# Kernel tuning notes

Hardware: AMD Instinct MI355X
Metric: run time of the kernel (lower is better)

The kernel has to match this reference:

```python
import jax, jax.numpy as jnp
import numpy as np

N_NODES = 50000
N_EDGES = 800000
IN_DIM = 128
HIDDEN = 128
OUT_DIM = 128


def setup_inputs() -> dict:
    key = jax.random.key(0)
    ks = jax.random.split(key, 16)
    s = 0.05
    inp = {
        "x": jax.random.normal(ks[0], (N_NODES, IN_DIM), jnp.float32),
        "edge_index": jax.random.randint(ks[1], (2, N_EDGES), 0, N_NODES, jnp.int64),
        "batch": jax.random.randint(ks[2], (25000,), 0, N_NODES, jnp.int64),
        "labels": jax.random.randint(ks[3], (N_NODES,), 0, 2, jnp.int64),
        # SAGEConv layer 1: in->hidden
        "W1l": jax.random.normal(ks[4], (HIDDEN, IN_DIM), jnp.float32) * s,
        "b1": jnp.zeros((HIDDEN,), jnp.float32),
        "W1r": jax.random.normal(ks[5], (HIDDEN, IN_DIM), jnp.float32) * s,
        # SAGEConv layer 2: hidden->hidden
        "W2l": jax.random.normal(ks[6], (HIDDEN, HIDDEN), jnp.float32) * s,
        "b2": jnp.zeros((HIDDEN,), jnp.float32),
        "W2r": jax.random.normal(ks[7], (HIDDEN, HIDDEN), jnp.float32) * s,
        # SAGEConv layer 3: hidden->out
        "W3l": jax.random.normal(ks[8], (OUT_DIM, HIDDEN), jnp.float32) * s,
        "b3": jnp.zeros((OUT_DIM,), jnp.float32),
        "W3r": jax.random.normal(ks[9], (OUT_DIM, HIDDEN), jnp.float32) * s,
        # classifier head: out->2
        "Wlin": jax.random.normal(ks[10], (2, OUT_DIM), jnp.float32) * s,
        "blin": jnp.zeros((2,), jnp.float32),
    }
    return inp


def _sage_conv(h, src, dst, Wl, bl, Wr):
    # mean aggregation of source features at destination nodes
    msg = h[src]                                            # [E, d]
    ssum = jax.ops.segment_sum(msg, dst, num_segments=N_NODES)
    cnt = jax.ops.segment_sum(jnp.ones((src.shape[0], 1), h.dtype), dst,
                              num_segments=N_NODES)
    agg = ssum / jnp.maximum(cnt, 1.0)
    # lin_l(agg) + lin_r(h): aggregate-then-transform (same math, cheaper)
    return agg @ Wl.T + bl + h @ Wr.T


def reference(x, edge_index, batch, labels,
              W1l, b1, W1r, W2l, b2, W2r, W3l, b3, W3r, Wlin, blin):
    src, dst = edge_index[0], edge_index[1]
    h = jax.nn.relu(_sage_conv(x, src, dst, W1l, b1, W1r))
    h = jax.nn.relu(_sage_conv(h, src, dst, W2l, b2, W2r))
    h = _sage_conv(h, src, dst, W3l, b3, W3r)               # no act after last
    preds = jax.nn.softmax(h @ Wlin.T + blin, axis=1)       # nn.Softmax(dim=1)
    # CrossEntropyLoss on (already-softmaxed) preds, as in the original module
    logp = jax.nn.log_softmax(preds[batch], axis=1)
    loss = -jnp.mean(jnp.take_along_axis(logp, labels[batch][:, None], axis=1))
    return loss
```

## Files before the change

### kernel.cpp

```cpp
#include <hip/hip_runtime.h>
#include <hip/hip_bf16.h>

#define N_NODES 50000
#define MPAD    50048
#define N_EDGES 800000
#define DIM     128
#define N_BATCH 25000
#define NBUCK   196
#define BCAP    8192
#define NBIN    64

typedef unsigned short u16;
typedef unsigned int   u32;
typedef unsigned char  u8;
typedef unsigned long long u64;

typedef __attribute__((ext_vector_type(8))) short bf16x8;
typedef __attribute__((ext_vector_type(4))) float f32x4;
typedef __attribute__((ext_vector_type(2))) float f32x2;

static __device__ __forceinline__ float bf2f(u16 u) {
    union { u32 i; float f; } v; v.i = ((u32)u) << 16; return v.f;
}
static __device__ __forceinline__ u16 f2bf(float f) {
    union { float f; u32 i; } v; v.f = f;
    u32 x = v.i;
    u32 r = x + 0x7fffu + ((x >> 16) & 1u);
    return (u16)(r >> 16);
}
template <bool HI>
static __device__ __forceinline__ u32 pk8(float a, float b, u32 old) {
    return (u32)__builtin_amdgcn_cvt_pk_fp8_f32(a, b, (int)old, HI);
}


__global__ void k_init(int* bcur, float* accum, int* hcount, u8* mask,
                       int* c1g, int* c3g, int* o1g, int* o3g) {
    int gid = blockIdx.x * 256 + threadIdx.x;
    if (gid < NBUCK) bcur[gid] = gid * BCAP;
    if (gid < NBIN) { c1g[gid] = 0; c3g[gid] = 0; o1g[gid] = 0; o3g[gid] = 0; }
    if (gid < N_NODES) mask[gid] = 0;
    if (gid == 0) { accum[0] = 0.f; hcount[0] = 0; }
}


#define SB_PART 196
#define SB_CX   3324
#define SB_CW   3708
#define SB_MK   3806

__global__ __launch_bounds__(256) void k_setup(
    const int* __restrict__ src, const int* __restrict__ dst,
    int* __restrict__ bcur, u64* __restrict__ ebuf,
    const float* __restrict__ x, u16* __restrict__ xb, u8* __restrict__ x8,
    const float* __restrict__ W1l, const float* __restrict__ W1r,
    const float* __restrict__ W2l, const float* __restrict__ W2r,
    const float* __restrict__ W3l, const float* __restrict__ W3r,
    u16* __restrict__ wout,
    const int* __restrict__ batch, u8* __restrict__ mask) {
    __shared__ int hist[NBUCK];
    __shared__ int lbase[NBUCK];
    __shared__ int gdelta[NBUCK];
    __shared__ u64 stage[4096];
    __shared__ int gaddr[4096];
    int bid = blockIdx.x;
    int t = threadIdx.x;

    if (bid < SB_PART) {
        for (int i = t; i < NBUCK; i += 256) hist[i] = 0;
        __syncthreads();

        int base = bid * 4096;
        int cnt = N_EDGES - base; if (cnt > 4096) cnt = 4096; if (cnt < 0) cnt = 0;

        int es[16], ed[16], rr[16];
#pragma unroll
        for (int k = 0; k < 16; ++k) {
            int i = t + (k << 8);
            bool ok = i < cnt;
            int e = ok ? (base + i) : 0;
            int s = src[e], d = dst[e];
            es[k] = s; ed[k] = d;
            int r = -1;
            if (ok) r = atomicAdd(&hist[d >> 8], 1);
            rr[k] = r;
        }
        __syncthreads();

        if (t < 64) {
            int run = 0;
            for (int c = 0; c < 4; ++c) {
                int idx = c * 64 + t;
                int v = (idx < NBUCK) ? hist[idx] : 0;
                int orig = v;
                for (int off = 1; off < 64; off <<= 1) {
                    int u = __shfl_up(v, off);
                    if (t >= off) v += u;
                }
                int tot = __shfl(v, 63);
                if (idx < NBUCK) lbase[idx] = run + v - orig;
                run += tot;
            }
        }
        __syncthreads();

        if (t < NBUCK) {
            int c = hist[t];
            int g = atomicAdd(&bcur[t], c);
            gdelta[t] = g - lbase[t];
        }
        __syncthreads();

#pragma unroll
        for (int k = 0; k < 16; ++k) {
            if (rr[k] >= 0) {
                int b = ed[k] >> 8;
                int slot = lbase[b] + rr[k];
                stage[slot] = (((u64)(u32)ed[k]) << 32) | (u32)es[k];
                gaddr[slot] = gdelta[b] + slot;
            }
        }
        __syncthreads();

        for (int i = t; i < cnt; i += 256) {
            ebuf[gaddr[i]] = stage[i];
        }
    } else if (bid < SB_CX) {
        int gid = (bid - SB_PART) * 256 + t;
        int row = gid >> 4;
        int c8  = (gid & 15) << 3;
        u32 outw[4];
        u32 w0 = 0, w1 = 0;
        if (row < N_NODES) {
            const float4* p = (const float4*)(x + (size_t)row * DIM + c8);
            float4 v0 = p[0], v1 = p[1];
            outw[0] = (u32)f2bf(v0.x) | ((u32)f2bf(v0.y) << 16);
            outw[1] = (u32)f2bf(v0.z) | ((u32)f2bf(v0.w) << 16);
            outw[2] = (u32)f2bf(v1.x) | ((u32)f2bf(v1.y) << 16);
            outw[3] = (u32)f2bf(v1.z) | ((u32)f2bf(v1.w) << 16);
            w0 = pk8<false>(v0.x, v0.y, 0); w0 = pk8<true>(v0.z, v0.w, w0);
            w1 = pk8<false>(v1.x, v1.y, 0); w1 = pk8<true>(v1.z, v1.w, w1);
        } else {
            outw[0] = outw[1] = outw[2] = outw[3] = 0;
        }
        *(uint4*)(xb + (size_t)row * DIM + c8) = *(uint4*)outw;
        uint2 o8; o8.x = w0; o8.y = w1;
        *(uint2*)(x8 + (size_t)row * DIM + c8) = o8;
    } else if (bid < SB_CW) {
        int i = (bid - SB_CX) * 256 + t;
        int mat = i >> 14, off = i & 16383;
        const float* s = (mat == 0) ? W1l : (mat == 1) ? W1r : (mat == 2) ? W2l
                       : (mat == 3) ? W2r : (mat == 4) ? W3l : W3r;
        wout[i] = f2bf(s[off]);
    } else {
        int s = (bid - SB_CW) * 256 + t;
        if (s < N_BATCH) mask[batch[s]] = 1;
    }
}


__global__ __launch_bounds__(256) void k_build(const u64* __restrict__ ebuf,
                                               const int* __restrict__ bcur,
                                               const u8* __restrict__ mask,
                                               int* __restrict__ row_ptr,
                                               int* __restrict__ deg,
                                               float* __restrict__ deg_inv,
                                               int* __restrict__ csr_src,
                                               int* __restrict__ c1g,
                                               int* __restrict__ c3g) {
    __shared__ int cnt256[256];
    __shared__ int sh[256];
    __shared__ int cur[256];
    __shared__ int bh1[NBIN];
    __shared__ int bh3[NBIN];
    __shared__ int shbase;
    int b  = blockIdx.x;
    int t  = threadIdx.x;
    int n0 = b << 8;
    cnt256[t] = 0;
    if (t < NBIN) { bh1[t] = 0; bh3[t] = 0; }
    if (t < 64) {
        int s = 0;
        for (int i = t; i < b; i += 64) s += bcur[i] - i * BCAP;
#pragma unroll
        for (int off = 32; off > 0; off >>= 1) s += __shfl_xor(s, off);
        if (t == 0) shbase = s;
    }
    __syncthreads();
    int bbase = shbase;

    int cnt = bcur[b] - b * BCAP;
    const u64* eb = ebuf + (size_t)b * BCAP;
    for (int i = t; i < cnt; i += 256) {
        int d = (int)(eb[i] >> 32);
        atomicAdd(&cnt256[d - n0], 1);
    }
    __syncthreads();

    int myc = cnt256[t];
    sh[t] = myc;
    __syncthreads();
    for (int off = 1; off < 256; off <<= 1) {
        int x = (t >= off) ? sh[t - off] : 0;
        __syncthreads();
        sh[t] += x;
        __syncthreads();
    }
    int rp = bbase + sh[t] - myc;
    int n  = n0 + t;
    if (n < N_NODES) {
        row_ptr[n] = rp;
        deg[n]     = myc;
        deg_inv[n] = 1.0f / (float)(myc < 1 ? 1 : myc);
        int bin = myc < NBIN ? myc : NBIN - 1;
        atomicAdd(&bh1[bin], 1);
        if (mask[n]) atomicAdd(&bh3[bin], 1);
    }
    cur[t] = rp;
    __syncthreads();

    for (int i = t; i < cnt; i += 256) {
        u64 p = eb[i];
        int d = (int)(p >> 32);
        int s = (int)(u32)p;
        int pos = atomicAdd(&cur[d - n0], 1);
        csr_src[pos] = s;
    }
    __syncthreads();
    if (t < NBIN) {
        if (bh1[t]) atomicAdd(&c1g[t], bh1[t]);
        if (bh3[t]) atomicAdd(&c3g[t], bh3[t]);
    }
}


__global__ __launch_bounds__(256) void k_dscatter(const int* __restrict__ deg,
                                                  const u8* __restrict__ mask,
                                                  const int* __restrict__ c1g,
                                                  const int* __restrict__ c3g,
                                                  int* __restrict__ o1g,
                                                  int* __restrict__ o3g,
                                                  int* __restrict__ wl1,
                                                  int* __restrict__ wl3,
                                                  int* __restrict__ n3) {
    __shared__ int bh1[NBIN], bh3[NBIN], bb1[NBIN], bb3[NBIN];
    int t = threadIdx.x;
    int n = blockIdx.x * 256 + t;
    if (t < NBIN) { bh1[t] = 0; bh3[t] = 0; }
    __syncthreads();
    bool valid = n < N_NODES;
    int d = 0, r1 = -1, r3 = -1;
    if (valid) {
        d = deg[n]; if (d >= NBIN) d = NBIN - 1;
        r1 = atomicAdd(&bh1[d], 1);
        if (mask[n]) r3 = atomicAdd(&bh3[d], 1);
    }
    __syncthreads();
    if (t < 64) {
        int v1 = c1g[t], v3 = c3g[t];
        int i1 = v1, i3 = v3;
        for (int off = 1; off < 64; off <<= 1) {
            int u1 = __shfl_up(i1, off);
            int u3 = __shfl_up(i3, off);
            if (t >= off) { i1 += u1; i3 += u3; }
        }
        int res1 = atomicAdd(&o1g[t], bh1[t]);
        int res3 = atomicAdd(&o3g[t], bh3[t]);
        bb1[t] = (i1 - v1) + res1;
        bb3[t] = (i3 - v3) + res3;
        if (blockIdx.x == 0 && t == 63) n3[0] = i3;
    }
    __syncthreads();
    if (valid) {
        wl1[bb1[d] + r1] = n;
        if (r3 >= 0) wl3[bb3[d] + r3] = n;
    }
}


template <bool RELU, bool PRUNED, bool W8>
__global__ __launch_bounds__(256) void k_sage(
    const u16* __restrict__ h, const u8* __restrict__ h8,
    const int* __restrict__ csr_src,
    const int* __restrict__ row_ptr, const int* __restrict__ deg,
    const float* __restrict__ deg_inv,
    const int* __restrict__ wl, const int* __restrict__ wlN,
    const u16* __restrict__ Wl, const u16* __restrict__ Wr,
    const float* __restrict__ bias, u16* __restrict__ out,
    u8* __restrict__ out8) {
    __shared__ u16 tile[16 * 128];
    __shared__ int wlid[16];
    int nwl = PRUNED ? wlN[0] : N_NODES;
    int m0  = blockIdx.x * 16;
    if (m0 >= nwl) return;

    int t    = threadIdx.x;
    int lane = t & 63;
    int wid  = t >> 6;
    int sub  = lane & 15;
    int grp  = lane >> 4;
    int nloc = (wid << 2) + grp;
    int gb   = lane & 48;
    int node = (m0 + nloc < nwl) ? wl[m0 + nloc] : -1;
    if (sub == 0) wlid[nloc] = node;

    float a0 = 0, a1 = 0, a2 = 0, a3 = 0, a4 = 0, a5 = 0, a6 = 0, a7 = 0;

#define ACC8(r) { f32x2 p; \
    p = __builtin_amdgcn_cvt_pk_f32_fp8((r).x, false); a0 += p[0]; a1 += p[1]; \
    p = __builtin_amdgcn_cvt_pk_f32_fp8((r).x, true);  a2 += p[0]; a3 += p[1]; \
    p = __builtin_amdgcn_cvt_pk_f32_fp8((r).y, false); a4 += p[0]; a5 += p[1]; \
    p = __builtin_amdgcn_cvt_pk_f32_fp8((r).y, true);  a6 += p[0]; a7 += p[1]; }

    if (node >= 0) {
        int start = row_ptr[node];
        int cnt   = deg[node];
        for (int c0 = 0; c0 < cnt; c0 += 16) {
            int rem = cnt - c0; if (rem > 16) rem = 16;
            int sidx = 0;
            if (sub < rem) sidx = csr_src[start + c0 + sub];
            int j = 0;
            for (; j + 8 <= rem; j += 8) {
                int i0 = __shfl(sidx, gb + j);
                int i1 = __shfl(sidx, gb + j + 1);
                int i2 = __shfl(sidx, gb + j + 2);
                int i3 = __shfl(sidx, gb + j + 3);
                int i4 = __shfl(sidx, gb + j + 4);
                int i5 = __shfl(sidx, gb + j + 5);
                int i6 = __shfl(sidx, gb + j + 6);
                int i7 = __shfl(sidx, gb + j + 7);
                uint2 r0 = *(const uint2*)(h8 + (size_t)i0 * DIM + sub * 8);
                uint2 r1 = *(const uint2*)(h8 + (size_t)i1 * DIM + sub * 8);
                uint2 r2 = *(const uint2*)(h8 + (size_t)i2 * DIM + sub * 8);
                uint2 r3 = *(const uint2*)(h8 + (size_t)i3 * DIM + sub * 8);
                uint2 r4 = *(const uint2*)(h8 + (size_t)i4 * DIM + sub * 8);
                uint2 r5 = *(const uint2*)(h8 + (size_t)i5 * DIM + sub * 8);
                uint2 r6 = *(const uint2*)(h8 + (size_t)i6 * DIM + sub * 8);
                uint2 r7 = *(const uint2*)(h8 + (size_t)i7 * DIM + sub * 8);
                ACC8(r0); ACC8(r1); ACC8(r2); ACC8(r3);
                ACC8(r4); ACC8(r5); ACC8(r6); ACC8(r7);
            }
            for (; j + 4 <= rem; j += 4) {
                int i0 = __shfl(sidx, gb + j);
                int i1 = __shfl(sidx, gb + j + 1);
                int i2 = __shfl(sidx, gb + j + 2);
                int i3 = __shfl(sidx, gb + j + 3);
                uint2 r0 = *(const uint2*)(h8 + (size_t)i0 * DIM + sub * 8);
                uint2 r1 = *(const uint2*)(h8 + (size_t)i1 * DIM + sub * 8);
                uint2 r2 = *(const uint2*)(h8 + (size_t)i2 * DIM + sub * 8);
                uint2 r3 = *(const uint2*)(h8 + (size_t)i3 * DIM + sub * 8);
                ACC8(r0); ACC8(r1); ACC8(r2); ACC8(r3);
            }
            for (; j < rem; ++j) {
                int i0 = __shfl(sidx, gb + j);
                uint2 r0 = *(const uint2*)(h8 + (size_t)i0 * DIM + sub * 8);
                ACC8(r0);
            }
        }
        float inv = deg_inv[node];
        a0 *= inv; a1 *= inv; a2 *= inv; a3 *= inv;
        a4 *= inv; a5 *= inv; a6 *= inv; a7 *= inv;
    }
#undef ACC8

    {
        uint4 o;
        o.x = (u32)f2bf(a0) | ((u32)f2bf(a1) << 16);
        o.y = (u32)f2bf(a2) | ((u32)f2bf(a3) << 16);
        o.z = (u32)f2bf(a4) | ((u32)f2bf(a5) << 16);
        o.w = (u32)f2bf(a6) | ((u32)f2bf(a7) << 16);
        int chunk = sub ^ (nloc & 7);
        *(uint4*)&tile[nloc * 128 + chunk * 8] = o;
    }
    __syncthreads();

    const int fr = sub;
    const int kq = grp << 3;
    bf16x8 aF0[4], aF1[4];
    int rnode = wlid[fr];
    int safe_r = rnode < 0 ? 0 : rnode;
    const u16* ph = h + (size_t)safe_r * DIM + kq;
#pragma unroll
    for (int kt = 0; kt < 4; ++kt) {
        int c = (grp + kt * 4) ^ (fr & 7);
        aF0[kt] = *(const bf16x8*)&tile[fr * 128 + c * 8];
        aF1[kt] = *(const bf16x8*)(ph + kt * 32);
    }
#pragma unroll
    for (int q = 0; q < 2; ++q) {
        int nt = wid * 2 + q;
        const u16* pwl = Wl + (size_t)(nt * 16 + fr) * DIM + kq;
        const u16* pwr = Wr + (size_t)(nt * 16 + fr) * DIM + kq;
        f32x4 acc = {0.f, 0.f, 0.f, 0.f};
#pragma unroll
        for (int kt = 0; kt < 4; ++kt) {
            bf16x8 w = *(const bf16x8*)(pwl + kt * 32);
            acc = __builtin_amdgcn_mfma_f32_16x16x32_bf16(aF0[kt], w, acc, 0, 0, 0);
        }
#pragma unroll
        for (int kt = 0; kt < 4; ++kt) {
            bf16x8 w = *(const bf16x8*)(pwr + kt * 32);
            acc = __builtin_amdgcn_mfma_f32_16x16x32_bf16(aF1[kt], w, acc, 0, 0, 0);
        }
        int col = nt * 16 + fr;
        float b = bias[col];
#pragma unroll
        for (int j = 0; j < 4; ++j) {
            int onode = wlid[(grp << 2) + j];
            if (onode >= 0) {
                float v = acc[j] + b;
                if (RELU) v = fmaxf(v, 0.f);
                out[(size_t)onode * DIM + col] = f2bf(v);
                if (W8) out8[(size_t)onode * DIM + col] = (u8)(pk8<false>(v, v, 0) & 0xffu);
            }
        }
    }
}


__global__ __launch_bounds__(256) void k_head(
    const u16* __restrict__ h3, const int* __restrict__ batch,
    const int* __restrict__ labels, const float* __restrict__ Wlin,
    const float* __restrict__ blin, float* __restrict__ accum,
    int* __restrict__ hcount, float* __restrict__ out) {
    __shared__ float wsh[256];
    __shared__ float red[4];
    int t = threadIdx.x;
    wsh[t] = Wlin[t];
    __syncthreads();

    int lane = t & 63;
    int g    = lane >> 4;
    int sub  = lane & 15;
    int wv   = (blockIdx.x * 256 + t) >> 6;
    int samp = wv * 4 + g;

    float contrib = 0.f;
    float z0 = 0.f, z1 = 0.f;
    int n = 0;
    if (samp < N_BATCH) {
        n = batch[samp];
        uint4 u = *(const uint4*)(h3 + (size_t)n * DIM + sub * 8);
        const u32* uw = (const u32*)&u;
        int cb = sub * 8;
#pragma unroll
        for (int q = 0; q < 4; ++q) {
            float hlo = bf2f((u16)(uw[q] & 0xffffu));
            float hhi = bf2f((u16)(uw[q] >> 16));
            z0 += hlo * wsh[cb + q * 2]       + hhi * wsh[cb + q * 2 + 1];
            z1 += hlo * wsh[128 + cb + q * 2] + hhi * wsh[128 + cb + q * 2 + 1];
        }
    }
#pragma unroll
    for (int off = 8; off > 0; off >>= 1) {
        z0 += __shfl_xor(z0, off);
        z1 += __shfl_xor(z1, off);
    }
    if (samp < N_BATCH) {
        z0 += blin[0]; z1 += blin[1];
        float m  = fmaxf(z0, z1);
        float e0 = expf(z0 - m), e1 = expf(z1 - m);
        float s  = e0 + e1;
        float p0 = e0 / s, p1 = e1 / s;
        float m2  = fmaxf(p0, p1);
        float lse = m2 + logf(expf(p0 - m2) + expf(p1 - m2));
        int lab = labels[n];
        float lp = ((lab == 0) ? p0 : p1) - lse;
        if (sub == 0) contrib = -lp * (1.0f / (float)N_BATCH);
    }
#pragma unroll
    for (int off = 16; off < 64; off <<= 1) contrib += __shfl_xor(contrib, off);
    if (lane == 0) red[t >> 6] = contrib;
    __syncthreads();
    if (t == 0) {
        atomicAdd(accum, red[0] + red[1] + red[2] + red[3]);
        __threadfence();
        int c = atomicAdd(hcount, 1);
        if (c == (int)gridDim.x - 1) {
            float v = atomicAdd(accum, 0.0f);
            out[0] = v;
        }
    }
}


extern "C" void kernel_launch(void* const* d_in, const int* in_sizes, int n_in,
                              void* d_out, int out_size, void* d_ws, size_t ws_size,
                              hipStream_t stream) {
    const float* x    = (const float*)d_in[0];
    const int*   eidx = (const int*)d_in[1];
    const int*   batch  = (const int*)d_in[2];
    const int*   labels = (const int*)d_in[3];
    const float* W1l = (const float*)d_in[4];
    const float* b1  = (const float*)d_in[5];
    const float* W1r = (const float*)d_in[6];
    const float* W2l = (const float*)d_in[7];
    const float* b2  = (const float*)d_in[8];
    const float* W2r = (const float*)d_in[9];
    const float* W3l = (const float*)d_in[10];
    const float* b3  = (const float*)d_in[11];
    const float* W3r = (const float*)d_in[12];
    const float* Wlin = (const float*)d_in[13];
    const float* blin = (const float*)d_in[14];

    const int* src = eidx;
    const int* dst = eidx + N_EDGES;

    size_t off = 0;
    auto alloc = [&](size_t bytes) -> char* {
        off = (off + 511) & ~(size_t)511;
        char* p = (char*)d_ws + off;
        off += bytes;
        return p;
    };
    int*   bcur    = (int*)  alloc(NBUCK * 4);
    int*   row_ptr = (int*)  alloc(N_NODES * 4);
    int*   deg     = (int*)  alloc(N_NODES * 4);
    float* deg_inv = (float*)alloc(N_NODES * 4);
    int*   csr_src = (int*)  alloc(N_EDGES * 4);
    u64*   ebuf    = (u64*)  alloc((size_t)NBUCK * BCAP * 8);
    u16*   wb      = (u16*)  alloc(6 * DIM * DIM * 2);
    u16*   xb      = (u16*)  alloc((size_t)MPAD * DIM * 2);
    u16*   bufA    = (u16*)  alloc((size_t)MPAD * DIM * 2);
    u8*    x8      = (u8*)   alloc((size_t)MPAD * DIM);
    u8*    a8      = (u8*)   alloc((size_t)MPAD * DIM);
    u8*    b8      = (u8*)   alloc((size_t)MPAD * DIM);
    u8*    mask    = (u8*)   alloc(N_NODES);
    int*   c1g     = (int*)  alloc(NBIN * 4);
    int*   c3g     = (int*)  alloc(NBIN * 4);
    int*   o1g     = (int*)  alloc(NBIN * 4);
    int*   o3g     = (int*)  alloc(NBIN * 4);
    int*   wl1     = (int*)  alloc(MPAD * 4);
    int*   wl3     = (int*)  alloc(MPAD * 4);
    int*   n3      = (int*)  alloc(4);
    float* accum   = (float*)alloc(4);
    int*   hcount  = (int*)  alloc(4);

    u16* bufB = xb;

    u16* w1l = wb + 0 * DIM * DIM;
    u16* w1r = wb + 1 * DIM * DIM;
    u16* w2l = wb + 2 * DIM * DIM;
    u16* w2r = wb + 3 * DIM * DIM;
    u16* w3l = wb + 4 * DIM * DIM;
    u16* w3r = wb + 5 * DIM * DIM;

    const int NB196 = (N_NODES + 255) / 256;
    const int SGB   = N_NODES / 16;
    const int HB2   = (N_BATCH + 15) / 16;

    k_init<<<NB196, 256, 0, stream>>>(bcur, accum, hcount, mask, c1g, c3g, o1g, o3g);
    k_setup<<<SB_MK, 256, 0, stream>>>(src, dst, bcur, ebuf,
                                       x, xb, x8,
                                       W1l, W1r, W2l, W2r, W3l, W3r, wb,
                                       batch, mask);
    k_build<<<NBUCK, 256, 0, stream>>>(ebuf, bcur, mask, row_ptr, deg,
                                       deg_inv, csr_src, c1g, c3g);
    k_dscatter<<<NB196, 256, 0, stream>>>(deg, mask, c1g, c3g, o1g, o3g,
                                          wl1, wl3, n3);

    k_sage<true, false, true><<<SGB, 256, 0, stream>>>(
        xb, x8, csr_src, row_ptr, deg, deg_inv, wl1, n3, w1l, w1r, b1, bufA, a8);
    k_sage<true, false, true><<<SGB, 256, 0, stream>>>(
        bufA, a8, csr_src, row_ptr, deg, deg_inv, wl1, n3, w2l, w2r, b2, bufB, b8);
    k_sage<false, true, false><<<SGB, 256, 0, stream>>>(
        bufB, b8, csr_src, row_ptr, deg, deg_inv, wl3, n3, w3l, w3r, b3, bufA, nullptr);

    k_head<<<HB2, 256, 0, stream>>>(bufA, batch, labels, Wlin, blin,
                                    accum, hcount, (float*)d_out);
}
```

Measured before the change: 191.1 us.

## Process 32 nodes per block with 16-byte fp8 gathers in SAGE kernel

Each 256-thread block now handles 32 destination nodes instead of 16. Eight lanes per node gather 16-byte fp8 rows instead of sixteen lanes gathering 8-byte rows, with packed f32x2 accumulation. The MFMA stage is remapped so each wave covers one 16-row tile and four of the eight output column tiles. The intent is wider memory transactions, more nodes in flight per block, and fewer blocks, at the cost of more LDS per block and a different wave-to-tile mapping.

Result: no change. 193.4 us (+1.2%).

```diff
diff --git a/kernel.cpp b/kernel.cpp
--- a/kernel.cpp
+++ b/kernel.cpp
@@ -288,107 +288,122 @@
     const u16* __restrict__ Wl, const u16* __restrict__ Wr,
     const float* __restrict__ bias, u16* __restrict__ out,
     u8* __restrict__ out8) {
-    __shared__ u16 tile[16 * 128];
-    __shared__ int wlid[16];
+    __shared__ u16 tile[32 * 128];
+    __shared__ int wlid[32];
     int nwl = PRUNED ? wlN[0] : N_NODES;
-    int m0  = blockIdx.x * 16;
+    int m0  = blockIdx.x * 32;
     if (m0 >= nwl) return;
 
     int t    = threadIdx.x;
     int lane = t & 63;
     int wid  = t >> 6;
-    int sub  = lane & 15;
-    int grp  = lane >> 4;
-    int nloc = (wid << 2) + grp;
-    int gb   = lane & 48;
+    int sub  = lane & 7;
+    int nloc = (wid << 3) + (lane >> 3);
+    int gb   = lane & 56;
     int node = (m0 + nloc < nwl) ? wl[m0 + nloc] : -1;
     if (sub == 0) wlid[nloc] = node;
 
-    float a0 = 0, a1 = 0, a2 = 0, a3 = 0, a4 = 0, a5 = 0, a6 = 0, a7 = 0;
-
-#define ACC8(r) { f32x2 p; \
-    p = __builtin_amdgcn_cvt_pk_f32_fp8((r).x, false); a0 += p[0]; a1 += p[1]; \
-    p = __builtin_amdgcn_cvt_pk_f32_fp8((r).x, true);  a2 += p[0]; a3 += p[1]; \
-    p = __builtin_amdgcn_cvt_pk_f32_fp8((r).y, false); a4 += p[0]; a5 += p[1]; \
-    p = __builtin_amdgcn_cvt_pk_f32_fp8((r).y, true);  a6 += p[0]; a7 += p[1]; }
+    f32x2 ac0 = {0,0}, ac1 = {0,0}, ac2 = {0,0}, ac3 = {0,0};
+    f32x2 ac4 = {0,0}, ac5 = {0,0}, ac6 = {0,0}, ac7 = {0,0};
+
+#define ACC16(r) { f32x2 p; \
+    p = __builtin_amdgcn_cvt_pk_f32_fp8((r).x, false); ac0 += p; \
+    p = __builtin_amdgcn_cvt_pk_f32_fp8((r).x, true);  ac1 += p; \
+    p = __builtin_amdgcn_cvt_pk_f32_fp8((r).y, false); ac2 += p; \
+    p = __builtin_amdgcn_cvt_pk_f32_fp8((r).y, true);  ac3 += p; \
+    p = __builtin_amdgcn_cvt_pk_f32_fp8((r).z, false); ac4 += p; \
+    p = __builtin_amdgcn_cvt_pk_f32_fp8((r).z, true);  ac5 += p; \
+    p = __builtin_amdgcn_cvt_pk_f32_fp8((r).w, false); ac6 += p; \
+    p = __builtin_amdgcn_cvt_pk_f32_fp8((r).w, true);  ac7 += p; }
 
     if (node >= 0) {
         int start = row_ptr[node];
         int cnt   = deg[node];
-        for (int c0 = 0; c0 < cnt; c0 += 16) {
-            int rem = cnt - c0; if (rem > 16) rem = 16;
+        for (int c0 = 0; c0 < cnt; c0 += 8) {
+            int rem = cnt - c0; if (rem > 8) rem = 8;
             int sidx = 0;
             if (sub < rem) sidx = csr_src[start + c0 + sub];
             int j = 0;
-            for (; j + 8 <= rem; j += 8) {
+            if (rem == 8) {
+                int i0 = __shfl(sidx, gb);
+                int i1 = __shfl(sidx, gb + 1);
+                int i2 = __shfl(sidx, gb + 2);
+                int i3 = __shfl(sidx, gb + 3);
+                int i4 = __shfl(sidx, gb + 4);
+                int i5 = __shfl(sidx, gb + 5);
+                int i6 = __shfl(sidx, gb + 6);
+                int i7 = __shfl(sidx, gb + 7);
+                uint4 r0 = *(const uint4*)(h8 + (size_t)i0 * DIM + sub * 16);
+                uint4 r1 = *(const uint4*)(h8 + (size_t)i1 * DIM + sub * 16);
+                uint4 r2 = *(const uint4*)(h8 + (size_t)i2 * DIM + sub * 16);
+                uint4 r3 = *(const uint4*)(h8 + (size_t)i3 * DIM + sub * 16);
+                uint4 r4 = *(const uint4*)(h8 + (size_t)i4 * DIM + sub * 16);
+                uint4 r5 = *(const uint4*)(h8 + (size_t)i5 * DIM + sub * 16);
+                uint4 r6 = *(const uint4*)(h8 + (size_t)i6 * DIM + sub * 16);
+                uint4 r7 = *(const uint4*)(h8 + (size_t)i7 * DIM + sub * 16);
+                ACC16(r0); ACC16(r1); ACC16(r2); ACC16(r3);
+                ACC16(r4); ACC16(r5); ACC16(r6); ACC16(r7);
+                j = 8;
+            }
+            if (j + 4 <= rem) {
                 int i0 = __shfl(sidx, gb + j);
                 int i1 = __shfl(sidx, gb + j + 1);
                 int i2 = __shfl(sidx, gb + j + 2);
                 int i3 = __shfl(sidx, gb + j + 3);
-                int i4 = __shfl(sidx, gb + j + 4);
-                int i5 = __shfl(sidx, gb + j + 5);
-                int i6 = __shfl(sidx, gb + j + 6);
-                int i7 = __shfl(sidx, gb + j + 7);
-                uint2 r0 = *(const uint2*)(h8 + (size_t)i0 * DIM + sub * 8);
-                uint2 r1 = *(const uint2*)(h8 + (size_t)i1 * DIM + sub * 8);
-                uint2 r2 = *(const uint2*)(h8 + (size_t)i2 * DIM + sub * 8);
-                uint2 r3 = *(const uint2*)(h8 + (size_t)i3 * DIM + sub * 8);
-                uint2 r4 = *(const uint2*)(h8 + (size_t)i4 * DIM + sub * 8);
-                uint2 r5 = *(const uint2*)(h8 + (size_t)i5 * DIM + sub * 8);
-                uint2 r6 = *(const uint2*)(h8 + (size_t)i6 * DIM + sub * 8);
-                uint2 r7 = *(const uint2*)(h8 + (size_t)i7 * DIM + sub * 8);
-                ACC8(r0); ACC8(r1); ACC8(r2); ACC8(r3);
-                ACC8(r4); ACC8(r5); ACC8(r6); ACC8(r7);
-            }
-            for (; j + 4 <= rem; j += 4) {
-                int i0 = __shfl(sidx, gb + j);
-                int i1 = __shfl(sidx, gb + j + 1);
-                int i2 = __shfl(sidx, gb + j + 2);
-                int i3 = __shfl(sidx, gb + j + 3);
-                uint2 r0 = *(const uint2*)(h8 + (size_t)i0 * DIM + sub * 8);
-                uint2 r1 = *(const uint2*)(h8 + (size_t)i1 * DIM + sub * 8);
-                uint2 r2 = *(const uint2*)(h8 + (size_t)i2 * DIM + sub * 8);
-                uint2 r3 = *(const uint2*)(h8 + (size_t)i3 * DIM + sub * 8);
-                ACC8(r0); ACC8(r1); ACC8(r2); ACC8(r3);
+                uint4 r0 = *(const uint4*)(h8 + (size_t)i0 * DIM + sub * 16);
+                uint4 r1 = *(const uint4*)(h8 + (size_t)i1 * DIM + sub * 16);
+                uint4 r2 = *(const uint4*)(h8 + (size_t)i2 * DIM + sub * 16);
+                uint4 r3 = *(const uint4*)(h8 + (size_t)i3 * DIM + sub * 16);
+                ACC16(r0); ACC16(r1); ACC16(r2); ACC16(r3);
+                j += 4;
             }
             for (; j < rem; ++j) {
                 int i0 = __shfl(sidx, gb + j);
-                uint2 r0 = *(const uint2*)(h8 + (size_t)i0 * DIM + sub * 8);
-                ACC8(r0);
+                uint4 r0 = *(const uint4*)(h8 + (size_t)i0 * DIM + sub * 16);
+                ACC16(r0);
             }
         }
         float inv = deg_inv[node];
-        a0 *= inv; a1 *= inv; a2 *= inv; a3 *= inv;
-        a4 *= inv; a5 *= inv; a6 *= inv; a7 *= inv;
-    }
-#undef ACC8
+        f32x2 vinv = {inv, inv};
+        ac0 *= vinv; ac1 *= vinv; ac2 *= vinv; ac3 *= vinv;
+        ac4 *= vinv; ac5 *= vinv; ac6 *= vinv; ac7 *= vinv;
+    }
+#undef ACC16
 
     {
-        uint4 o;
-        o.x = (u32)f2bf(a0) | ((u32)f2bf(a1) << 16);
-        o.y = (u32)f2bf(a2) | ((u32)f2bf(a3) << 16);
-        o.z = (u32)f2bf(a4) | ((u32)f2bf(a5) << 16);
-        o.w = (u32)f2bf(a6) | ((u32)f2bf(a7) << 16);
-        int chunk = sub ^ (nloc & 7);
-        *(uint4*)&tile[nloc * 128 + chunk * 8] = o;
-    }
-    __syncthreads();
-
-    const int fr = sub;
-    const int kq = grp << 3;
+        uint4 oA, oB;
+        oA.x = (u32)f2bf(ac0[0]) | ((u32)f2bf(ac0[1]) << 16);
+        oA.y = (u32)f2bf(ac1[0]) | ((u32)f2bf(ac1[1]) << 16);
+        oA.z = (u32)f2bf(ac2[0]) | ((u32)f2bf(ac2[1]) << 16);
+        oA.w = (u32)f2bf(ac3[0]) | ((u32)f2bf(ac3[1]) << 16);
+        oB.x = (u32)f2bf(ac4[0]) | ((u32)f2bf(ac4[1]) << 16);
+        oB.y = (u32)f2bf(ac5[0]) | ((u32)f2bf(ac5[1]) << 16);
+        oB.z = (u32)f2bf(ac6[0]) | ((u32)f2bf(ac6[1]) << 16);
+        oB.w = (u32)f2bf(ac7[0]) | ((u32)f2bf(ac7[1]) << 16);
+        int cA = (sub * 2)     ^ (nloc & 7);
+        int cB = (sub * 2 + 1) ^ (nloc & 7);
+        *(uint4*)&tile[nloc * 128 + cA * 8] = oA;
+        *(uint4*)&tile[nloc * 128 + cB * 8] = oB;
+    }
+    __syncthreads();
+
+    const int fr  = lane & 15;
+    const int grp = lane >> 4;
+    const int kq  = grp << 3;
+    const int rt  = wid & 1;
     bf16x8 aF0[4], aF1[4];
-    int rnode = wlid[fr];
+    int rnode = wlid[rt * 16 + fr];
     int safe_r = rnode < 0 ? 0 : rnode;
     const u16* ph = h + (size_t)safe_r * DIM + kq;
 #pragma unroll
     for (int kt = 0; kt < 4; ++kt) {
         int c = (grp + kt * 4) ^ (fr & 7);
-        aF0[kt] = *(const bf16x8*)&tile[fr * 128 + c * 8];
+        aF0[kt] = *(const bf16x8*)&tile[(rt * 16 + fr) * 128 + c * 8];
         aF1[kt] = *(const bf16x8*)(ph + kt * 32);
     }
 #pragma unroll
-    for (int q = 0; q < 2; ++q) {
-        int nt = wid * 2 + q;
+    for (int q = 0; q < 4; ++q) {
+        int nt = (wid >> 1) * 4 + q;
         const u16* pwl = Wl + (size_t)(nt * 16 + fr) * DIM + kq;
         const u16* pwr = Wr + (size_t)(nt * 16 + fr) * DIM + kq;
         f32x4 acc = {0.f, 0.f, 0.f, 0.f};
@@ -406,7 +421,7 @@
         float b = bias[col];
 #pragma unroll
         for (int j = 0; j < 4; ++j) {
-            int onode = wlid[(grp << 2) + j];
+            int onode = wlid[rt * 16 + (grp << 2) + j];
             if (onode >= 0) {
                 float v = acc[j] + b;
                 if (RELU) v = fmaxf(v, 0.f);
@@ -546,7 +561,7 @@
     u16* w3r = wb + 5 * DIM * DIM;
 
     const int NB196 = (N_NODES + 255) / 256;
-    const int SGB   = N_NODES / 16;
+    const int SGB   = (N_NODES + 31) / 32;
     const int HB2   = (N_BATCH + 15) / 16;
 
     k_init<<<NB196, 256, 0, stream>>>(bcur, accum, hcount, mask, c1g, c3g, o1g, o3g);
```

## Fuse classifier head into last SAGE layer, replace init kernel with memset

Applied to the files above, without the earlier changes.

Removes k_init and zeroes a contiguous scratch region (batch multiplicity counts, bucket cursors, bin counters, accumulators) with a single async memset. The batch mask becomes a per-node multiplicity count, so the last SAGE layer computes the loss directly for each needed node, weighted by how often that node appears in the batch. This removes the separate k_head kernel and the write and reread of the final hidden features. Labels are passed through the out8 pointer and the head contains dead duplicated code, which makes it fragile. Note that blin is not added in the branch that actually produces the loss.

After: 196.9 us. +3.0%, slower.

```diff
diff --git a/kernel.cpp b/kernel.cpp
--- a/kernel.cpp
+++ b/kernel.cpp
@@ -34,16 +34,6 @@
 }
 
 
-__global__ void k_init(int* bcur, float* accum, int* hcount, u8* mask,
-                       int* c1g, int* c3g, int* o1g, int* o3g) {
-    int gid = blockIdx.x * 256 + threadIdx.x;
-    if (gid < NBUCK) bcur[gid] = gid * BCAP;
-    if (gid < NBIN) { c1g[gid] = 0; c3g[gid] = 0; o1g[gid] = 0; o3g[gid] = 0; }
-    if (gid < N_NODES) mask[gid] = 0;
-    if (gid == 0) { accum[0] = 0.f; hcount[0] = 0; }
-}
-
-
 #define SB_PART 196
 #define SB_CX   3324
 #define SB_CW   3708
@@ -57,7 +47,7 @@
     const float* __restrict__ W2l, const float* __restrict__ W2r,
     const float* __restrict__ W3l, const float* __restrict__ W3r,
     u16* __restrict__ wout,
-    const int* __restrict__ batch, u8* __restrict__ mask) {
+    const int* __restrict__ batch, int* __restrict__ mult) {
     __shared__ int hist[NBUCK];
     __shared__ int lbase[NBUCK];
     __shared__ int gdelta[NBUCK];
@@ -107,7 +97,7 @@
         if (t < NBUCK) {
             int c = hist[t];
             int g = atomicAdd(&bcur[t], c);
-            gdelta[t] = g - lbase[t];
+            gdelta[t] = t * BCAP + g - lbase[t];
         }
         __syncthreads();
 
@@ -154,14 +144,14 @@
         wout[i] = f2bf(s[off]);
     } else {
         int s = (bid - SB_CW) * 256 + t;
-        if (s < N_BATCH) mask[batch[s]] = 1;
+        if (s < N_BATCH) atomicAdd(&mult[batch[s]], 1);
     }
 }
 
 
 __global__ __launch_bounds__(256) void k_build(const u64* __restrict__ ebuf,
                                                const int* __restrict__ bcur,
-                                               const u8* __restrict__ mask,
+                                               const int* __restrict__ mult,
                                                int* __restrict__ row_ptr,
                                                int* __restrict__ deg,
                                                float* __restrict__ deg_inv,
@@ -181,7 +171,7 @@
     if (t < NBIN) { bh1[t] = 0; bh3[t] = 0; }
     if (t < 64) {
         int s = 0;
-        for (int i = t; i < b; i += 64) s += bcur[i] - i * BCAP;
+        for (int i = t; i < b; i += 64) s += bcur[i];
 #pragma unroll
         for (int off = 32; off > 0; off >>= 1) s += __shfl_xor(s, off);
         if (t == 0) shbase = s;
@@ -189,7 +179,7 @@
     __syncthreads();
     int bbase = shbase;
 
-    int cnt = bcur[b] - b * BCAP;
+    int cnt = bcur[b];
     const u64* eb = ebuf + (size_t)b * BCAP;
     for (int i = t; i < cnt; i += 256) {
         int d = (int)(eb[i] >> 32);
@@ -214,7 +204,7 @@
         deg_inv[n] = 1.0f / (float)(myc < 1 ? 1 : myc);
         int bin = myc < NBIN ? myc : NBIN - 1;
         atomicAdd(&bh1[bin], 1);
-        if (mask[n]) atomicAdd(&bh3[bin], 1);
+        if (mult[n]) atomicAdd(&bh3[bin], 1);
     }
     cur[t] = rp;
     __syncthreads();
@@ -235,7 +225,7 @@
 
 
 __global__ __launch_bounds__(256) void k_dscatter(const int* __restrict__ deg,
-                                                  const u8* __restrict__ mask,
+                                                  const int* __restrict__ mult,
                                                   const int* __restrict__ c1g,
                                                   const int* __restrict__ c3g,
                                                   int* __restrict__ o1g,
@@ -253,7 +243,7 @@
     if (valid) {
         d = deg[n]; if (d >= NBIN) d = NBIN - 1;
         r1 = atomicAdd(&bh1[d], 1);
-        if (mask[n]) r3 = atomicAdd(&bh3[d], 1);
+        if (mult[n]) r3 = atomicAdd(&bh3[d], 1);
     }
     __syncthreads();
     if (t < 64) {
@@ -278,7 +268,7 @@
 }
 
 
-template <bool RELU, bool PRUNED, bool W8>
+template <bool RELU, bool HEAD>
 __global__ __launch_bounds__(256) void k_sage(
     const u16* __restrict__ h, const u8* __restrict__ h8,
     const int* __restrict__ csr_src,
@@ -287,10 +277,16 @@
     const int* __restrict__ wl, const int* __restrict__ wlN,
     const u16* __restrict__ Wl, const u16* __restrict__ Wr,
     const float* __restrict__ bias, u16* __restrict__ out,
-    u8* __restrict__ out8) {
+    u8* __restrict__ out8,
+    const int* __restrict__ mult, const float* __restrict__ Wlin,
+    const float* __restrict__ blin, float* __restrict__ accum,
+    int* __restrict__ hcount, float* __restrict__ lossout) {
     __shared__ u16 tile[16 * 128];
     __shared__ int wlid[16];
-    int nwl = PRUNED ? wlN[0] : N_NODES;
+    __shared__ float wsh[256];
+    __shared__ float red[4];
+    __shared__ int wmult[16];
+    int nwl = HEAD ? wlN[0] : N_NODES;
     int m0  = blockIdx.x * 16;
     if (m0 >= nwl) return;
 
@@ -302,7 +298,11 @@
     int nloc = (wid << 2) + grp;
     int gb   = lane & 48;
     int node = (m0 + nloc < nwl) ? wl[m0 + nloc] : -1;
-    if (sub == 0) wlid[nloc] = node;
+    if (sub == 0) {
+        wlid[nloc] = node;
+        if (HEAD) wmult[nloc] = (node >= 0) ? mult[node] : 0;
+    }
+    if (HEAD) wsh[t] = Wlin[t];
 
     float a0 = 0, a1 = 0, a2 = 0, a3 = 0, a4 = 0, a5 = 0, a6 = 0, a7 = 0;
 
@@ -386,6 +386,7 @@
         aF0[kt] = *(const bf16x8*)&tile[fr * 128 + c * 8];
         aF1[kt] = *(const bf16x8*)(ph + kt * 32);
     }
+    if (HEAD) __syncthreads();
 #pragma unroll
     for (int q = 0; q < 2; ++q) {
         int nt = wid * 2 + q;
@@ -406,79 +407,79 @@
         float b = bias[col];
 #pragma unroll
         for (int j = 0; j < 4; ++j) {
-            int onode = wlid[(grp << 2) + j];
-            if (onode >= 0) {
-                float v = acc[j] + b;
-                if (RELU) v = fmaxf(v, 0.f);
-                out[(size_t)onode * DIM + col] = f2bf(v);
-                if (W8) out8[(size_t)onode * DIM + col] = (u8)(pk8<false>(v, v, 0) & 0xffu);
-            }
-        }
-    }
-}
-
-
-__global__ __launch_bounds__(256) void k_head(
-    const u16* __restrict__ h3, const int* __restrict__ batch,
-    const int* __restrict__ labels, const float* __restrict__ Wlin,
-    const float* __restrict__ blin, float* __restrict__ accum,
-    int* __restrict__ hcount, float* __restrict__ out) {
-    __shared__ float wsh[256];
-    __shared__ float red[4];
-    int t = threadIdx.x;
-    wsh[t] = Wlin[t];
-    __syncthreads();
-
-    int lane = t & 63;
-    int g    = lane >> 4;
-    int sub  = lane & 15;
-    int wv   = (blockIdx.x * 256 + t) >> 6;
-    int samp = wv * 4 + g;
-
-    float contrib = 0.f;
-    float z0 = 0.f, z1 = 0.f;
-    int n = 0;
-    if (samp < N_BATCH) {
-        n = batch[samp];
-        uint4 u = *(const uint4*)(h3 + (size_t)n * DIM + sub * 8);
-        const u32* uw = (const u32*)&u;
-        int cb = sub * 8;
-#pragma unroll
-        for (int q = 0; q < 4; ++q) {
-            float hlo = bf2f((u16)(uw[q] & 0xffffu));
-            float hhi = bf2f((u16)(uw[q] >> 16));
-            z0 += hlo * wsh[cb + q * 2]       + hhi * wsh[cb + q * 2 + 1];
-            z1 += hlo * wsh[128 + cb + q * 2] + hhi * wsh[128 + cb + q * 2 + 1];
-        }
-    }
-#pragma unroll
-    for (int off = 8; off > 0; off >>= 1) {
-        z0 += __shfl_xor(z0, off);
-        z1 += __shfl_xor(z1, off);
-    }
-    if (samp < N_BATCH) {
-        z0 += blin[0]; z1 += blin[1];
-        float m  = fmaxf(z0, z1);
-        float e0 = expf(z0 - m), e1 = expf(z1 - m);
-        float s  = e0 + e1;
-        float p0 = e0 / s, p1 = e1 / s;
-        float m2  = fmaxf(p0, p1);
-        float lse = m2 + logf(expf(p0 - m2) + expf(p1 - m2));
-        int lab = labels[n];
-        float lp = ((lab == 0) ? p0 : p1) - lse;
-        if (sub == 0) contrib = -lp * (1.0f / (float)N_BATCH);
-    }
-#pragma unroll
-    for (int off = 16; off < 64; off <<= 1) contrib += __shfl_xor(contrib, off);
-    if (lane == 0) red[t >> 6] = contrib;
-    __syncthreads();
-    if (t == 0) {
-        atomicAdd(accum, red[0] + red[1] + red[2] + red[3]);
-        __threadfence();
-        int c = atomicAdd(hcount, 1);
-        if (c == (int)gridDim.x - 1) {
-            float v = atomicAdd(accum, 0.0f);
-            out[0] = v;
+            int oidx = (grp << 2) + j;
+            int onode = wlid[oidx];
+            float v = acc[j] + b;
+            if (RELU) v = fmaxf(v, 0.f);
+            u16 vb = f2bf(v);
+            if (HEAD) {
+                tile[oidx * 128 + col] = vb;
+            } else if (onode >= 0) {
+                out[(size_t)onode * DIM + col] = vb;
+                out8[(size_t)onode * DIM + col] = (u8)(pk8<false>(v, v, 0) & 0xffu);
+            }
+        }
+    }
+
+    if (HEAD) {
+        __syncthreads();
+        int wnode = wlid[nloc];
+        float z0 = 0.f, z1 = 0.f;
+        {
+            uint4 u = *(const uint4*)&tile[nloc * 128 + sub * 8];
+            const u32* uw = (const u32*)&u;
+            int cb = sub * 8;
+#pragma unroll
+            for (int q = 0; q < 4; ++q) {
+                float hlo = bf2f((u16)(uw[q] & 0xffffu));
+                float hhi = bf2f((u16)(uw[q] >> 16));
+                z0 += hlo * wsh[cb + q * 2]       + hhi * wsh[cb + q * 2 + 1];
+                z1 += hlo * wsh[128 + cb + q * 2] + hhi * wsh[128 + cb + q * 2 + 1];
+            }
+        }
+#pragma unroll
+        for (int off = 8; off > 0; off >>= 1) {
+            z0 += __shfl_xor(z0, off);
+            z1 += __shfl_xor(z1, off);
+        }
+        float contrib = 0.f;
+        if (sub == 0 && wnode >= 0) {
+            z0 += blin[0]; z1 += blin[1];
+            float m  = fmaxf(z0, z1);
+            float e0 = expf(z0 - m), e1 = expf(z1 - m);
+            float s  = e0 + e1;
+            float p0 = e0 / s, p1 = e1 / s;
+            float m2  = fmaxf(p0, p1);
+            float lse = m2 + logf(expf(p0 - m2) + expf(p1 - m2));
+            float lp = ((wmult[nloc] == 0) ? p0 : p0);
+            (void)lp;
+            contrib = 0.f;
+        }
+        if (sub == 0 && wnode >= 0) {
+            float m  = fmaxf(z0, z1);
+            float e0 = expf(z0 - m), e1 = expf(z1 - m);
+            float s  = e0 + e1;
+            float p0 = e0 / s, p1 = e1 / s;
+            float m2  = fmaxf(p0, p1);
+            float lse = m2 + logf(expf(p0 - m2) + expf(p1 - m2));
+            int lab = ((const int*)hcount)[0] == -12345 ? 0 : 0;
+            (void)lab;
+            int label = ((const int*)out8)[wnode];
+            float lpv = ((label == 0) ? p0 : p1) - lse;
+            contrib = -lpv * (float)wmult[nloc] * (1.0f / (float)N_BATCH);
+        }
+#pragma unroll
+        for (int off = 16; off < 64; off <<= 1) contrib += __shfl_xor(contrib, off);
+        if (lane == 0) red[wid] = contrib;
+        __syncthreads();
+        if (t == 0) {
+            atomicAdd(accum, red[0] + red[1] + red[2] + red[3]);
+            __threadfence();
+            int nactive = (nwl + 15) >> 4;
+            int c = atomicAdd(hcount, 1);
+            if (c == nactive - 1) {
+                lossout[0] = atomicAdd(accum, 0.0f);
+            }
         }
     }
 }
@@ -513,7 +514,17 @@
         off += bytes;
         return p;
     };
-    int*   bcur    = (int*)  alloc(NBUCK * 4);
+    char* zbase = alloc((size_t)MPAD * 4 + NBUCK * 4 + 4 * NBIN * 4 + 8);
+    int*   mult   = (int*)zbase;
+    int*   bcur   = mult + MPAD;
+    int*   c1g    = bcur + NBUCK;
+    int*   c3g    = c1g + NBIN;
+    int*   o1g    = c3g + NBIN;
+    int*   o3g    = o1g + NBIN;
+    float* accum  = (float*)(o3g + NBIN);
+    int*   hcount = (int*)(accum + 1);
+    size_t zbytes = (size_t)MPAD * 4 + NBUCK * 4 + 4 * NBIN * 4 + 8;
+
     int*   row_ptr = (int*)  alloc(N_NODES * 4);
     int*   deg     = (int*)  alloc(N_NODES * 4);
     float* deg_inv = (float*)alloc(N_NODES * 4);
@@ -525,16 +536,9 @@
     u8*    x8      = (u8*)   alloc((size_t)MPAD * DIM);
     u8*    a8      = (u8*)   alloc((size_t)MPAD * DIM);
     u8*    b8      = (u8*)   alloc((size_t)MPAD * DIM);
-    u8*    mask    = (u8*)   alloc(N_NODES);
-    int*   c1g     = (int*)  alloc(NBIN * 4);
-    int*   c3g     = (int*)  alloc(NBIN * 4);
-    int*   o1g     = (int*)  alloc(NBIN * 4);
-    int*   o3g     = (int*)  alloc(NBIN * 4);
     int*   wl1     = (int*)  alloc(MPAD * 4);
     int*   wl3     = (int*)  alloc(MPAD * 4);
     int*   n3      = (int*)  alloc(4);
-    float* accum   = (float*)alloc(4);
-    int*   hcount  = (int*)  alloc(4);
 
     u16* bufB = xb;
 
@@ -547,25 +551,24 @@
 
     const int NB196 = (N_NODES + 255) / 256;
     const int SGB   = N_NODES / 16;
-    const int HB2   = (N_BATCH + 15) / 16;
-
-    k_init<<<NB196, 256, 0, stream>>>(bcur, accum, hcount, mask, c1g, c3g, o1g, o3g);
+
+    hipMemsetAsync(zbase, 0, zbytes, stream);
     k_setup<<<SB_MK, 256, 0, stream>>>(src, dst, bcur, ebuf,
                                        x, xb, x8,
                                        W1l, W1r, W2l, W2r, W3l, W3r, wb,
-                                       batch, mask);
-    k_build<<<NBUCK, 256, 0, stream>>>(ebuf, bcur, mask, row_ptr, deg,
+                                       batch, mult);
+    k_build<<<NBUCK, 256, 0, stream>>>(ebuf, bcur, mult, row_ptr, deg,
                                        deg_inv, csr_src, c1g, c3g);
-    k_dscatter<<<NB196, 256, 0, stream>>>(deg, mask, c1g, c3g, o1g, o3g,
+    k_dscatter<<<NB196, 256, 0, stream>>>(deg, mult, c1g, c3g, o1g, o3g,
                                           wl1, wl3, n3);
 
-    k_sage<true, false, true><<<SGB, 256, 0, stream>>>(
-        xb, x8, csr_src, row_ptr, deg, deg_inv, wl1, n3, w1l, w1r, b1, bufA, a8);
-    k_sage<true, false, true><<<SGB, 256, 0, stream>>>(
-        bufA, a8, csr_src, row_ptr, deg, deg_inv, wl1, n3, w2l, w2r, b2, bufB, b8);
-    k_sage<false, true, false><<<SGB, 256, 0, stream>>>(
-        bufB, b8, csr_src, row_ptr, deg, deg_inv, wl3, n3, w3l, w3r, b3, bufA, nullptr);
-
-    k_head<<<HB2, 256, 0, stream>>>(bufA, batch, labels, Wlin, blin,
-                                    accum, hcount, (float*)d_out);
-}
+    k_sage<true, false><<<SGB, 256, 0, stream>>>(
+        xb, x8, csr_src, row_ptr, deg, deg_inv, wl1, n3, w1l, w1r, b1, bufA, a8,
+        nullptr, nullptr, nullptr, nullptr, nullptr, nullptr);
+    k_sage<true, false><<<SGB, 256, 0, stream>>>(
+        bufA, a8, csr_src, row_ptr, deg, deg_inv, wl1, n3, w2l, w2r, b2, bufB, b8,
+        nullptr, nullptr, nullptr, nullptr, nullptr, nullptr);
+    k_sage<false, true><<<SGB, 256, 0, stream>>>(
+        bufB, b8, csr_src, row_ptr, deg, deg_inv, wl3, n3, w3l, w3r, b3, bufA,
+        (u8*)labels, mult, Wlin, blin, accum, hcount, (float*)d_out);
+}
```
